# Kernel optimization log

Hardware: AMD Instinct MI355X
Metric: run time of the kernel (lower is better)

Reference implementation:

```python
import jax, jax.numpy as jnp
import numpy as np

BITS = 8
EPS = 1e-5


def round_clip(x, lo, hi):
    # round-then-clip with straight-through estimator (matches Audyn's round_clip)
    return x + jax.lax.stop_gradient(jnp.clip(jnp.round(x), lo, hi) - x)


def setup_inputs() -> dict:
    key = jax.random.key(0)
    kx, kw = jax.random.split(key)
    B, S, D_IN, D_OUT = 4, 2048, 4096, 16384
    x = jax.random.normal(kx, (B, S, D_IN), dtype=jnp.float32)
    # kaiming-uniform-ish scale: bound = 1/sqrt(in_features)
    bound = 1.0 / np.sqrt(D_IN)
    weight = jax.random.uniform(kw, (D_OUT, D_IN), dtype=jnp.float32,
                                minval=-bound, maxval=bound)
    return {"x": x, "weight": weight}


def reference(x, weight):
    q = float(2 ** (BITS - 1))  # 128
    # activation quantization: per-tensor abs-max
    gamma = jnp.maximum(jnp.max(jnp.abs(x)), EPS)
    xq = round_clip(x * (q / gamma), -q, q - 1.0)
    # weight quantization: per-tensor mean-abs (NB: source divides abs_weight, not weight)
    abs_w = jnp.abs(weight)
    beta = jnp.maximum(jnp.mean(abs_w), EPS)
    wq = round_clip(abs_w / beta, -1.0, 1.0)
    # GEMM (no bias: source always registers bias as None) + rescale
    y = jnp.einsum("bsd,od->bso", xq, wq)
    return y * (beta * gamma / q)
```

## Files before the change

### kernel.cpp

```cpp
#include <hip/hip_runtime.h>

typedef float f32x4 __attribute__((ext_vector_type(4)));
typedef int   i32x4 __attribute__((ext_vector_type(4)));
typedef char  s8x16 __attribute__((ext_vector_type(16)));

#define GAS __attribute__((address_space(1)))
#define LAS __attribute__((address_space(3)))

constexpr int M = 8192;
constexpr int N = 16384;
constexpr int K = 4096;
constexpr long long NX = (long long)M * K;
constexpr long long NW = (long long)N * K;
constexpr int NPART = 2048;


__global__ void reduce_absmax_kernel(const float* __restrict__ x,
                                     unsigned* __restrict__ gmax, int n4) {
  float m = 0.f;
  int stride = gridDim.x * blockDim.x;
  for (int i = blockIdx.x * blockDim.x + threadIdx.x; i < n4; i += stride) {
    f32x4 v = *(const f32x4*)(x + (size_t)i * 4);
    m = fmaxf(m, fmaxf(fmaxf(fabsf(v[0]), fabsf(v[1])),
                       fmaxf(fabsf(v[2]), fabsf(v[3]))));
  }
#pragma unroll
  for (int off = 32; off > 0; off >>= 1) m = fmaxf(m, __shfl_down(m, off));
  __shared__ float sm[4];
  int lane = threadIdx.x & 63, wid = threadIdx.x >> 6;
  if (lane == 0) sm[wid] = m;
  __syncthreads();
  if (threadIdx.x == 0) {
    m = fmaxf(fmaxf(sm[0], sm[1]), fmaxf(sm[2], sm[3]));
    atomicMax(gmax, __float_as_uint(m));
  }
}

__global__ void reduce_abssum_kernel(const float* __restrict__ w,
                                     float* __restrict__ partials, int n4) {
  float s = 0.f;
  int stride = gridDim.x * blockDim.x;
  for (int i = blockIdx.x * blockDim.x + threadIdx.x; i < n4; i += stride) {
    f32x4 v = *(const f32x4*)(w + (size_t)i * 4);
    s += fabsf(v[0]) + fabsf(v[1]) + fabsf(v[2]) + fabsf(v[3]);
  }
#pragma unroll
  for (int off = 32; off > 0; off >>= 1) s += __shfl_down(s, off);
  __shared__ float sm[4];
  int lane = threadIdx.x & 63, wid = threadIdx.x >> 6;
  if (lane == 0) sm[wid] = s;
  __syncthreads();
  if (threadIdx.x == 0) partials[blockIdx.x] = (sm[0] + sm[1]) + (sm[2] + sm[3]);
}

__global__ void finalize_kernel(const unsigned* __restrict__ gbits,
                                const float* __restrict__ partials,
                                float* __restrict__ params) {
  __shared__ double sd[256];
  double s = 0.0;
  for (int i = threadIdx.x; i < NPART; i += 256) s += (double)partials[i];
  sd[threadIdx.x] = s;
  __syncthreads();
  for (int h = 128; h > 0; h >>= 1) {
    if (threadIdx.x < h) sd[threadIdx.x] += sd[threadIdx.x + h];
    __syncthreads();
  }
  if (threadIdx.x == 0) {
    float beta  = fmaxf((float)(sd[0] / (double)NW), 1e-5f);
    float gamma = fmaxf(__uint_as_float(gbits[0]), 1e-5f);
    params[0] = 128.0f / gamma;
    params[1] = beta;
    params[2] = beta * gamma / 128.0f;
  }
}


__global__ void quant_x_kernel(const float* __restrict__ x,
                               char* __restrict__ xq,
                               const float* __restrict__ params, int n16) {
  float s = params[0];
  int stride = gridDim.x * blockDim.x;
  for (int i = blockIdx.x * blockDim.x + threadIdx.x; i < n16; i += stride) {
    const f32x4* p = (const f32x4*)(x + (size_t)i * 16);
    s8x16 o;
#pragma unroll
    for (int v = 0; v < 4; ++v) {
      f32x4 t = p[v];
#pragma unroll
      for (int k = 0; k < 4; ++k) {
        float r = fminf(fmaxf(rintf(t[k] * s), -128.f), 127.f);
        o[v * 4 + k] = (char)(int)r;
      }
    }
    *(s8x16*)(xq + (size_t)i * 16) = o;
  }
}

__global__ void quant_w_kernel(const float* __restrict__ w,
                               char* __restrict__ wq,
                               const float* __restrict__ params, int n16) {
  float beta = params[1];
  int stride = gridDim.x * blockDim.x;
  for (int i = blockIdx.x * blockDim.x + threadIdx.x; i < n16; i += stride) {
    const f32x4* p = (const f32x4*)(w + (size_t)i * 16);
    s8x16 o;
#pragma unroll
    for (int v = 0; v < 4; ++v) {
      f32x4 t = p[v];
#pragma unroll
      for (int k = 0; k < 4; ++k) {
        o[v * 4 + k] = (rintf(fabsf(t[k]) / beta) >= 1.0f) ? (char)1 : (char)0;
      }
    }
    *(s8x16*)(wq + (size_t)i * 16) = o;
  }
}


__global__ __launch_bounds__(256) void gemm_kernel(
    const char* __restrict__ A,
    const char* __restrict__ B,
    float* __restrict__ C,
    const float* __restrict__ params) {
  __shared__ __align__(16) char As[128 * 64];
  __shared__ __align__(16) char Bs[128 * 64];

  const int tid  = threadIdx.x;
  const int lane = tid & 63, wid = tid >> 6;
  const int wr = wid >> 1, wc = wid & 1;
  const int r16 = lane & 15, q4 = lane >> 4;
  const int m0 = blockIdx.y * 128, n0 = blockIdx.x * 128;
  const float sc = params[2];

  const int i0 = tid, i1 = 256 + tid;
  const char* ga0 = A + (size_t)(m0 + (i0 >> 2)) * K + (i0 & 3) * 16;
  const char* ga1 = A + (size_t)(m0 + (i1 >> 2)) * K + (i1 & 3) * 16;
  const char* gb0 = B + (size_t)(n0 + (i0 >> 2)) * K + (i0 & 3) * 16;
  const char* gb1 = B + (size_t)(n0 + (i1 >> 2)) * K + (i1 & 3) * 16;
  char* la0 = &As[i0 * 16];
  char* la1 = &As[i1 * 16];
  char* lb0 = &Bs[i0 * 16];
  char* lb1 = &Bs[i1 * 16];

  int aoff[4], boff[4];
#pragma unroll
  for (int i = 0; i < 4; ++i) {
    aoff[i] = (wr * 64 + i * 16 + r16) * 64 + q4 * 16;
    boff[i] = (wc * 64 + i * 16 + r16) * 64 + q4 * 16;
  }

  i32x4 acc[4][4] = {};

  for (int kt = 0; kt < K / 64; ++kt) {
    const int ko = kt * 64;
    __builtin_amdgcn_global_load_lds((const GAS void*)(ga0 + ko), (LAS void*)la0, 16, 0, 0);
    __builtin_amdgcn_global_load_lds((const GAS void*)(ga1 + ko), (LAS void*)la1, 16, 0, 0);
    __builtin_amdgcn_global_load_lds((const GAS void*)(gb0 + ko), (LAS void*)lb0, 16, 0, 0);
    __builtin_amdgcn_global_load_lds((const GAS void*)(gb1 + ko), (LAS void*)lb1, 16, 0, 0);
    __syncthreads();

    i32x4 af[4], bf[4];
#pragma unroll
    for (int i = 0; i < 4; ++i) af[i] = *(const i32x4*)&As[aoff[i]];
#pragma unroll
    for (int j = 0; j < 4; ++j) bf[j] = *(const i32x4*)&Bs[boff[j]];
#pragma unroll
    for (int i = 0; i < 4; ++i)
#pragma unroll
      for (int j = 0; j < 4; ++j)
        acc[i][j] = __builtin_amdgcn_mfma_i32_16x16x64_i8(af[i], bf[j], acc[i][j], 0, 0, 0);
    __syncthreads();
  }

  const int crow = m0 + wr * 64 + q4 * 4;
  const int ccol = n0 + wc * 64 + r16;
#pragma unroll
  for (int i = 0; i < 4; ++i)
#pragma unroll
    for (int j = 0; j < 4; ++j)
#pragma unroll
      for (int r = 0; r < 4; ++r)
        C[(size_t)(crow + i * 16 + r) * N + (ccol + j * 16)] = (float)acc[i][j][r] * sc;
}


extern "C" void kernel_launch(void* const* d_in, const int* in_sizes, int n_in,
                              void* d_out, int out_size, void* d_ws, size_t ws_size,
                              hipStream_t stream) {
  const float* x = (const float*)d_in[0];
  const float* w = (const float*)d_in[1];
  float* out = (float*)d_out;
  char* ws = (char*)d_ws;

  unsigned* gamma_bits = (unsigned*)ws;
  float*    params     = (float*)(ws + 16);
  float*    partials   = (float*)(ws + 256);
  char*     xq = ws + 16384;
  char*     wq = ws + 16384 + (size_t)NX;

  hipMemsetAsync(ws, 0, 256, stream);

  reduce_absmax_kernel<<<NPART, 256, 0, stream>>>(x, gamma_bits, (int)(NX / 4));
  reduce_abssum_kernel<<<NPART, 256, 0, stream>>>(w, partials, (int)(NW / 4));
  finalize_kernel<<<1, 256, 0, stream>>>(gamma_bits, partials, params);
  quant_x_kernel<<<2048, 256, 0, stream>>>(x, xq, params, (int)(NX / 16));
  quant_w_kernel<<<2048, 256, 0, stream>>>(w, wq, params, (int)(NW / 16));

  dim3 grid(N / 128, M / 128);
  gemm_kernel<<<grid, 256, 0, stream>>>(xq, wq, out, params);
}
```

Baseline: 863.4 us.

## Rewrite int8 GEMM with 256x256 tiles, triple-buffered swizzled LDS and pre-packed B

The GEMM moves from a 128x128 tile with 4 waves and single-buffered LDS to a 256x256 tile with 8 waves. A is staged through a triple-buffered, XOR-swizzled LDS ring, while B is repacked by the weight quantizer into an MFMA-fragment-major layout and read straight into registers, double-buffered across K steps. The kernel also adds a swizzled block-to-tile mapping for cache locality, explicit waitcnt and sched barriers, and setprio around the MFMA bursts. The aim is to raise arithmetic intensity and overlap memory loads with MFMA work, at the cost of more registers, 96 KB of LDS per block and fragile hand-tuned wait counts.

```diff
diff --git a/kernel.cpp b/kernel.cpp
--- a/kernel.cpp
+++ b/kernel.cpp
@@ -6,6 +6,7 @@
 
 #define GAS __attribute__((address_space(1)))
 #define LAS __attribute__((address_space(3)))
+#define SBAR __builtin_amdgcn_sched_barrier(0)
 
 constexpr int M = 8192;
 constexpr int N = 16384;
@@ -13,6 +14,7 @@
 constexpr long long NX = (long long)M * K;
 constexpr long long NW = (long long)N * K;
 constexpr int NPART = 2048;
+constexpr int NKT = 32;
 
 
 __global__ void reduce_absmax_kernel(const float* __restrict__ x,
@@ -97,85 +99,150 @@
 }
 
 __global__ void quant_w_kernel(const float* __restrict__ w,
-                               char* __restrict__ wq,
-                               const float* __restrict__ params, int n16) {
+                               char* __restrict__ wq2,
+                               const float* __restrict__ params, int nchunks) {
   float beta = params[1];
   int stride = gridDim.x * blockDim.x;
-  for (int i = blockIdx.x * blockDim.x + threadIdx.x; i < n16; i += stride) {
-    const f32x4* p = (const f32x4*)(w + (size_t)i * 16);
+  for (int u = blockIdx.x * blockDim.x + threadIdx.x; u < nchunks; u += stride) {
+    const int nr16 = u >> 12;
+    const int kc   = (u >> 4) & 255;
+    const int r16  = u & 15;
+    const float* src = w + (size_t)(nr16 * 16 + r16) * K + kc * 16;
     s8x16 o;
 #pragma unroll
     for (int v = 0; v < 4; ++v) {
-      f32x4 t = p[v];
-#pragma unroll
-      for (int k = 0; k < 4; ++k) {
+      f32x4 t = *(const f32x4*)(src + v * 4);
+#pragma unroll
+      for (int k = 0; k < 4; ++k)
         o[v * 4 + k] = (rintf(fabsf(t[k]) / beta) >= 1.0f) ? (char)1 : (char)0;
-      }
     }
-    *(s8x16*)(wq + (size_t)i * 16) = o;
-  }
-}
-
-
-__global__ __launch_bounds__(256) void gemm_kernel(
+    *(s8x16*)(wq2 + (size_t)u * 16) = o;
+  }
+}
+
+
+__global__ __launch_bounds__(512) void gemm_kernel(
     const char* __restrict__ A,
-    const char* __restrict__ B,
+    const char* __restrict__ Bq,
     float* __restrict__ C,
     const float* __restrict__ params) {
-  __shared__ __align__(16) char As[128 * 64];
-  __shared__ __align__(16) char Bs[128 * 64];
+  __shared__ __align__(16) char lds[98304];
 
   const int tid  = threadIdx.x;
   const int lane = tid & 63, wid = tid >> 6;
-  const int wr = wid >> 1, wc = wid & 1;
+  const int wm = wid >> 2, wn = wid & 3;
   const int r16 = lane & 15, q4 = lane >> 4;
-  const int m0 = blockIdx.y * 128, n0 = blockIdx.x * 128;
+
+  const int wg = (blockIdx.x & 7) * 256 + (blockIdx.x >> 3);
+  const int c  = wg >> 8, l = wg & 255;
+  const int m0 = (c * 4 + (l & 3)) * 256;
+  const int n0 = (l >> 2) * 256;
+
+  const int csw = ((lane & 7) ^ ((lane >> 3) & 7)) * 16;
+  const char* gA = A + (size_t)(m0 + wid * 32 + (lane >> 3)) * K + csw;
+  const int dA = wid * 4096 + lane * 16;
+
+#define STAGE_A(T, SLOTOFF) do { \
+    char* Lp = lds + (SLOTOFF); \
+    const char* ap = gA + (size_t)(T) * 128; \
+    __builtin_amdgcn_global_load_lds((const GAS void*)(ap),           (LAS void*)(Lp + dA),        16, 0, 0); \
+    __builtin_amdgcn_global_load_lds((const GAS void*)(ap +  8 * K),  (LAS void*)(Lp + dA + 1024), 16, 0, 0); \
+    __builtin_amdgcn_global_load_lds((const GAS void*)(ap + 16 * K),  (LAS void*)(Lp + dA + 2048), 16, 0, 0); \
+    __builtin_amdgcn_global_load_lds((const GAS void*)(ap + 24 * K),  (LAS void*)(Lp + dA + 3072), 16, 0, 0); \
+  } while (0)
+
+  const int nb16 = (n0 >> 4) + wn * 4;
+  const char* bB = Bq + ((size_t)(nb16 * 256 + q4) * 16 + r16) * 16;
+
+#define LOAD_B(T, BF) do { \
+    const char* bp = bB + (size_t)(T) * 2048; \
+    BF[0] = *(const i32x4*)(bp); \
+    BF[1] = *(const i32x4*)(bp + 65536); \
+    BF[2] = *(const i32x4*)(bp + 131072); \
+    BF[3] = *(const i32x4*)(bp + 196608); \
+    BF[4] = *(const i32x4*)(bp + 1024); \
+    BF[5] = *(const i32x4*)(bp + 65536 + 1024); \
+    BF[6] = *(const i32x4*)(bp + 131072 + 1024); \
+    BF[7] = *(const i32x4*)(bp + 196608 + 1024); \
+  } while (0)
+
+  const int abase = (wm * 128 + r16) * 128;
+  const int sw0 = ((q4) ^ (r16 & 7)) * 16;
+  const int sw1 = ((4 + q4) ^ (r16 & 7)) * 16;
+
+  i32x4 acc[8][4] = {};
+
+#define COMPUTE(BF, SLOTOFF) do { \
+    const char* bufp = lds + (SLOTOFF); \
+    i32x4 af[8]; \
+    _Pragma("unroll") \
+    for (int i = 0; i < 8; ++i) af[i] = *(const i32x4*)(bufp + abase + i * 2048 + sw0); \
+    __builtin_amdgcn_s_setprio(1); \
+    _Pragma("unroll") \
+    for (int i = 0; i < 8; ++i) { \
+      acc[i][0] = __builtin_amdgcn_mfma_i32_16x16x64_i8(af[i], BF[0], acc[i][0], 0, 0, 0); \
+      acc[i][1] = __builtin_amdgcn_mfma_i32_16x16x64_i8(af[i], BF[1], acc[i][1], 0, 0, 0); \
+      acc[i][2] = __builtin_amdgcn_mfma_i32_16x16x64_i8(af[i], BF[2], acc[i][2], 0, 0, 0); \
+      acc[i][3] = __builtin_amdgcn_mfma_i32_16x16x64_i8(af[i], BF[3], acc[i][3], 0, 0, 0); \
+    } \
+    __builtin_amdgcn_s_setprio(0); \
+    _Pragma("unroll") \
+    for (int i = 0; i < 8; ++i) af[i] = *(const i32x4*)(bufp + abase + i * 2048 + sw1); \
+    __builtin_amdgcn_s_setprio(1); \
+    _Pragma("unroll") \
+    for (int i = 0; i < 8; ++i) { \
+      acc[i][0] = __builtin_amdgcn_mfma_i32_16x16x64_i8(af[i], BF[4], acc[i][0], 0, 0, 0); \
+      acc[i][1] = __builtin_amdgcn_mfma_i32_16x16x64_i8(af[i], BF[5], acc[i][1], 0, 0, 0); \
+      acc[i][2] = __builtin_amdgcn_mfma_i32_16x16x64_i8(af[i], BF[6], acc[i][2], 0, 0, 0); \
+      acc[i][3] = __builtin_amdgcn_mfma_i32_16x16x64_i8(af[i], BF[7], acc[i][3], 0, 0, 0); \
+    } \
+    __builtin_amdgcn_s_setprio(0); \
+  } while (0)
+
+  i32x4 bfE[8], bfO[8];
+
+  STAGE_A(0, 0); SBAR;
+  STAGE_A(1, 32768); SBAR;
+  LOAD_B(0, bfE); SBAR;
+  asm volatile("s_waitcnt vmcnt(12)" ::: "memory");
+  SBAR;
+
+  int rc = 0;
+  for (int tt = 0; tt < 15; ++tt) {
+    const int t = tt * 2;
+    int rs = rc + 2; if (rs >= 3) rs -= 3;
+    __builtin_amdgcn_s_barrier(); SBAR;
+    STAGE_A(t + 2, rs * 32768); SBAR;
+    LOAD_B(t + 1, bfO); SBAR;
+    COMPUTE(bfE, rc * 32768);
+    SBAR;
+    asm volatile("s_waitcnt vmcnt(12)" ::: "memory");
+    SBAR;
+    rc = rc + 1; if (rc >= 3) rc -= 3;
+    rs = rc + 2; if (rs >= 3) rs -= 3;
+    __builtin_amdgcn_s_barrier(); SBAR;
+    STAGE_A(t + 3, rs * 32768); SBAR;
+    LOAD_B(t + 2, bfE); SBAR;
+    COMPUTE(bfO, rc * 32768);
+    SBAR;
+    asm volatile("s_waitcnt vmcnt(12)" ::: "memory");
+    SBAR;
+    rc = rc + 1; if (rc >= 3) rc -= 3;
+  }
+  __builtin_amdgcn_s_barrier(); SBAR;
+  LOAD_B(31, bfO); SBAR;
+  COMPUTE(bfE, 0);
+  SBAR;
+  asm volatile("s_waitcnt vmcnt(8)" ::: "memory");
+  SBAR;
+  __builtin_amdgcn_s_barrier(); SBAR;
+  COMPUTE(bfO, 32768);
+
   const float sc = params[2];
-
-  const int i0 = tid, i1 = 256 + tid;
-  const char* ga0 = A + (size_t)(m0 + (i0 >> 2)) * K + (i0 & 3) * 16;
-  const char* ga1 = A + (size_t)(m0 + (i1 >> 2)) * K + (i1 & 3) * 16;
-  const char* gb0 = B + (size_t)(n0 + (i0 >> 2)) * K + (i0 & 3) * 16;
-  const char* gb1 = B + (size_t)(n0 + (i1 >> 2)) * K + (i1 & 3) * 16;
-  char* la0 = &As[i0 * 16];
-  char* la1 = &As[i1 * 16];
-  char* lb0 = &Bs[i0 * 16];
-  char* lb1 = &Bs[i1 * 16];
-
-  int aoff[4], boff[4];
-#pragma unroll
-  for (int i = 0; i < 4; ++i) {
-    aoff[i] = (wr * 64 + i * 16 + r16) * 64 + q4 * 16;
-    boff[i] = (wc * 64 + i * 16 + r16) * 64 + q4 * 16;
-  }
-
-  i32x4 acc[4][4] = {};
-
-  for (int kt = 0; kt < K / 64; ++kt) {
-    const int ko = kt * 64;
-    __builtin_amdgcn_global_load_lds((const GAS void*)(ga0 + ko), (LAS void*)la0, 16, 0, 0);
-    __builtin_amdgcn_global_load_lds((const GAS void*)(ga1 + ko), (LAS void*)la1, 16, 0, 0);
-    __builtin_amdgcn_global_load_lds((const GAS void*)(gb0 + ko), (LAS void*)lb0, 16, 0, 0);
-    __builtin_amdgcn_global_load_lds((const GAS void*)(gb1 + ko), (LAS void*)lb1, 16, 0, 0);
-    __syncthreads();
-
-    i32x4 af[4], bf[4];
-#pragma unroll
-    for (int i = 0; i < 4; ++i) af[i] = *(const i32x4*)&As[aoff[i]];
-#pragma unroll
-    for (int j = 0; j < 4; ++j) bf[j] = *(const i32x4*)&Bs[boff[j]];
-#pragma unroll
-    for (int i = 0; i < 4; ++i)
-#pragma unroll
-      for (int j = 0; j < 4; ++j)
-        acc[i][j] = __builtin_amdgcn_mfma_i32_16x16x64_i8(af[i], bf[j], acc[i][j], 0, 0, 0);
-    __syncthreads();
-  }
-
-  const int crow = m0 + wr * 64 + q4 * 4;
-  const int ccol = n0 + wc * 64 + r16;
-#pragma unroll
-  for (int i = 0; i < 4; ++i)
+  const int crow = m0 + wm * 128 + q4 * 4;
+  const int ccol = n0 + wn * 64 + r16;
+#pragma unroll
+  for (int i = 0; i < 8; ++i)
 #pragma unroll
     for (int j = 0; j < 4; ++j)
 #pragma unroll
@@ -195,8 +262,8 @@
   unsigned* gamma_bits = (unsigned*)ws;
   float*    params     = (float*)(ws + 16);
   float*    partials   = (float*)(ws + 256);
-  char*     xq = ws + 16384;
-  char*     wq = ws + 16384 + (size_t)NX;
+  char*     xq  = ws + 16384;
+  char*     wq2 = ws + 16384 + (size_t)NX;
 
   hipMemsetAsync(ws, 0, 256, stream);
 
@@ -204,8 +271,7 @@
   reduce_abssum_kernel<<<NPART, 256, 0, stream>>>(w, partials, (int)(NW / 4));
   finalize_kernel<<<1, 256, 0, stream>>>(gamma_bits, partials, params);
   quant_x_kernel<<<2048, 256, 0, stream>>>(x, xq, params, (int)(NX / 16));
-  quant_w_kernel<<<2048, 256, 0, stream>>>(w, wq, params, (int)(NW / 16));
-
-  dim3 grid(N / 128, M / 128);
-  gemm_kernel<<<grid, 256, 0, stream>>>(xq, wq, out, params);
-}
+  quant_w_kernel<<<4096, 256, 0, stream>>>(w, wq2, params, (int)(NW / 16));
+
+  gemm_kernel<<<2048, 512, 0, stream>>>(xq, wq2, out, params);
+}
```

Result: faster. 803.7 us (-6.9%).
